# Kernel tuning notes

Measured on AMD Instinct MI355X. Metric: run time of the kernel, lower is better.

The kernel has to match this reference:

```python
import jax, jax.numpy as jnp
import numpy as np

EMBED_DIM = 128
NUM_HEADS = 16
D_K = EMBED_DIM // NUM_HEADS  # must equal n_wires = 8


def setup_inputs() -> dict:
    key = jax.random.key(0)
    k1, k2 = jax.random.split(key)
    x = jax.random.normal(k1, (8, 2048, EMBED_DIM), dtype=jnp.float32)
    theta = jax.random.normal(k2, (D_K,), dtype=jnp.float32)  # trainable RX angles, one per wire
    return {"x": x, "theta": theta}


def _quantum_measure(q, theta):
    # q: [B, H, S, 8]. RX(x)RX(theta) = RX(x+theta); product state gives <Z_i> = cos(phi_i).
    # CNOT chain C(0,1)..C(6,7),C(7,0) in Heisenberg picture:
    #   <Z_0> = prod_{i=1..7} cos(phi_i);  <Z_w> = prod_{i=0..w} cos(phi_i), w>=1.
    c = jnp.cos(q + theta)                       # [B,H,S,8]
    cp = jnp.cumprod(c, axis=-1)                 # prefix products prod_{0..w}
    z0 = jnp.prod(c[..., 1:], axis=-1, keepdims=True)
    return jnp.concatenate([z0, cp[..., 1:]], axis=-1)  # [B,H,S,8]


def reference(x, theta):
    B, S, E = x.shape
    # split heads: [B,S,E] -> [B,H,S,d_k]
    q = x.reshape(B, S, NUM_HEADS, D_K).transpose(0, 2, 1, 3)
    out = _quantum_measure(q, theta)             # [B,H,S,8]
    # merge heads back: [B,S,E]
    out = out.transpose(0, 2, 1, 3).reshape(B, S, E)
    scores = jnp.einsum('bse,bte->bst', out, out) / jnp.sqrt(jnp.float32(D_K))
    attn = jax.nn.softmax(scores, axis=-1)       # dropout = identity in eval mode
    return jnp.einsum('bst,bte->bse', attn, out)
```

## Files before the change

### kernel.cpp

```cpp
#include <hip/hip_runtime.h>

#define NB 8
#define SS 2048
#define DD 128
#define SCALE2 0.5101817664764817f
#define NEGINF -3.0e38f

typedef _Float16 f16x8 __attribute__((ext_vector_type(8)));
typedef float f32x16 __attribute__((ext_vector_type(16)));
typedef unsigned short u16;
typedef u16 u16x8 __attribute__((ext_vector_type(8)));
typedef unsigned int u32;

__device__ __forceinline__ u32 pkrtz(float a, float b) {
    u32 w;
    asm("v_cvt_pkrtz_f16_f32 %0, %1, %2" : "=v"(w) : "v"(a), "v"(b));
    return w;
}

__device__ __forceinline__ void gload_lds16(const u16* g, u16* l) {
    __builtin_amdgcn_global_load_lds(
        (const __attribute__((address_space(1))) unsigned*)g,
        (__attribute__((address_space(3))) unsigned*)l, 16, 0, 0);
}

__global__ __launch_bounds__(512) void qmeasure_kernel(const float* __restrict__ x,
                                                       const float* __restrict__ theta,
                                                       u16* __restrict__ G1,
                                                       u16* __restrict__ G2) {
    __shared__ u16 olds[32][136];
    const int bid = blockIdx.x;
    const int b = bid & 7;
    const int t = bid >> 3;
    const int tid = threadIdx.x;
    const int s = tid >> 4;
    const int c = tid & 15;

    float th[8];
    *(float4*)th = *(const float4*)theta;
    *(float4*)(th + 4) = *(const float4*)(theta + 4);

    const float* xp = x + (((size_t)b * SS + t * 32 + s) * DD) + c * 8;
    float4 a = *(const float4*)xp;
    float4 a2 = *(const float4*)(xp + 4);
    float cc[8];
    cc[0] = __cosf(a.x + th[0]);  cc[1] = __cosf(a.y + th[1]);
    cc[2] = __cosf(a.z + th[2]);  cc[3] = __cosf(a.w + th[3]);
    cc[4] = __cosf(a2.x + th[4]); cc[5] = __cosf(a2.y + th[5]);
    cc[6] = __cosf(a2.z + th[6]); cc[7] = __cosf(a2.w + th[7]);
    float o[8];
    o[1] = cc[0] * cc[1];
    o[2] = o[1] * cc[2]; o[3] = o[2] * cc[3]; o[4] = o[3] * cc[4];
    o[5] = o[4] * cc[5]; o[6] = o[5] * cc[6]; o[7] = o[6] * cc[7];
    float z = cc[1] * cc[2]; z *= cc[3]; z *= cc[4]; z *= cc[5]; z *= cc[6]; z *= cc[7];
    o[0] = z;

    u16x8 w;
#pragma unroll
    for (int e = 0; e < 8; ++e) w[e] = __builtin_bit_cast(u16, (_Float16)o[e]);
    *(u16x8*)&olds[s][c * 8] = w;
    __syncthreads();

    {
        const int kc = tid >> 6, hh = (tid >> 5) & 1, r = tid & 31;
        u16x8 g;
#pragma unroll
        for (int u = 0; u < 8; ++u) g[u] = olds[r][kc * 16 + hh * 8 + u];
        *(u16x8*)(G1 + (size_t)b * (SS * DD) + ((size_t)t * 512 + tid) * 8) = g;
    }
    {
        const int lo5 = tid & 31;
        const int hh = (tid >> 5) & 1;
        const int dkc = tid >> 6;
        const int dt = dkc >> 1, kc2 = dkc & 1;
        u16x8 g;
#pragma unroll
        for (int u = 0; u < 8; ++u) g[u] = olds[kc2 * 16 + hh * 8 + u][dt * 32 + lo5];
        const int chunk = t * 512 + dkc * 64 + hh * 32 + lo5;
        *(u16x8*)(G2 + (size_t)b * (SS * DD) + (size_t)chunk * 8) = g;
    }
}

__global__ __launch_bounds__(512, 2) void qattn_kernel(const u16* __restrict__ G1g,
                                                       const u16* __restrict__ G2g,
                                                       float* __restrict__ out) {
    __shared__ __align__(16) u16 sb[2][2][4][4096];

    const int tid = threadIdx.x;
    const int lane = tid & 63;
    const int wave = tid >> 6;
    const int lo5 = lane & 31;
    const int hi = lane >> 5;
    const int qw = wave & 1;
    const int kq = wave >> 1;
    const int bid = blockIdx.x;
    const int b = bid & 7;
    const int qg = bid >> 3;

    const u16* G1b = G1g + (size_t)b * (SS * DD);
    const u16* G2b = G2g + (size_t)b * (SS * DD);
    const u16* sbase = (qw ? G2b : G1b);

    f16x8 qf[8];
    {
        const u16* qp = G1b + (size_t)(qg * 2 + qw) * 4096 + lane * 8;
#pragma unroll
        for (int kc = 0; kc < 8; ++kc) qf[kc] = *(const f16x8*)(qp + kc * 512);
    }

#pragma unroll
    for (int pb = 0; pb < 2; ++pb) {
        const u16* src = sbase + (size_t)(kq * 16 + pb) * 4096 + lane * 8;
        u16* dst = &sb[pb][qw][kq][0];
#pragma unroll
        for (int w = 0; w < 8; ++w) gload_lds16(src + w * 512, dst + w * 512);
    }

    f32x16 accT[4];
#pragma unroll
    for (int dt = 0; dt < 4; ++dt)
#pragma unroll
        for (int e = 0; e < 16; ++e) accT[dt][e] = 0.f;
    float m = NEGINF, l = 0.f;

    for (int it = 0; it < 16; ++it) {
        const int cur = it & 1;
        if (it < 15) asm volatile("s_waitcnt vmcnt(8)" ::: "memory");
        else         asm volatile("s_waitcnt vmcnt(0)" ::: "memory");
        __builtin_amdgcn_sched_barrier(0);
        __builtin_amdgcn_s_barrier();
        __builtin_amdgcn_sched_barrier(0);

        const u16* Kb = &sb[cur][0][kq][0] + lane * 8;
        const u16* Vb = &sb[cur][1][kq][0] + lane * 8;

        f32x16 acA, acB;
#pragma unroll
        for (int e = 0; e < 16; ++e) { acA[e] = 0.f; acB[e] = 0.f; }
        __builtin_amdgcn_s_setprio(1);
#pragma unroll
        for (int kc = 0; kc < 4; ++kc) {
            f16x8 kf = *(const f16x8*)(Kb + kc * 512);
            acA = __builtin_amdgcn_mfma_f32_32x32x16_f16(kf, qf[kc], acA, 0, 0, 0);
        }
#pragma unroll
        for (int kc = 4; kc < 8; ++kc) {
            f16x8 kf = *(const f16x8*)(Kb + kc * 512);
            acB = __builtin_amdgcn_mfma_f32_32x32x16_f16(kf, qf[kc], acB, 0, 0, 0);
        }
        __builtin_amdgcn_s_setprio(0);
        f32x16 acc = acA + acB;

        f16x8 vf[8];
#pragma unroll
        for (int j = 0; j < 8; ++j) vf[j] = *(const f16x8*)(Vb + j * 512);

        float ma = fmaxf(fmaxf(acc[0], acc[1]), acc[2]);
        float mb = fmaxf(fmaxf(acc[8], acc[9]), acc[10]);
        ma = fmaxf(fmaxf(ma, acc[3]), acc[4]);
        mb = fmaxf(fmaxf(mb, acc[11]), acc[12]);
        ma = fmaxf(fmaxf(ma, acc[5]), acc[6]);
        mb = fmaxf(fmaxf(mb, acc[13]), acc[14]);
        ma = fmaxf(fmaxf(ma, acc[7]), mb);
        float tmax = fmaxf(ma, acc[15]) * SCALE2;
        tmax = fmaxf(tmax, __shfl_xor(tmax, 32));
        if (!__all(tmax <= m + 8.f)) {
            const float mnew = fmaxf(m, tmax);
            const float corr = exp2f(m - mnew);
            l *= corr;
#pragma unroll
            for (int dt = 0; dt < 4; ++dt)
#pragma unroll
                for (int e = 0; e < 16; ++e) accT[dt][e] *= corr;
            m = mnew;
        }
#pragma unroll
        for (int r = 0; r < 16; ++r) acc[r] = exp2f(acc[r] * SCALE2 - m);
        float s0 = (acc[0] + acc[1]) + (acc[2] + acc[3]);
        float s1 = (acc[4] + acc[5]) + (acc[6] + acc[7]);
        float s2 = (acc[8] + acc[9]) + (acc[10] + acc[11]);
        float s3 = (acc[12] + acc[13]) + (acc[14] + acc[15]);
        float rowsum = (s0 + s1) + (s2 + s3);
        rowsum += __shfl_xor(rowsum, 32);
        l += rowsum;

        f16x8 pa[2];
#pragma unroll
        for (int kc2 = 0; kc2 < 2; ++kc2) {
            const int r0 = kc2 * 8;
            u32 w0 = pkrtz(acc[r0 + 0], acc[r0 + 1]);
            u32 w2 = pkrtz(acc[r0 + 4], acc[r0 + 5]);
            asm("v_permlane32_swap_b32 %0, %1" : "+v"(w0), "+v"(w2));
            u32 w1 = pkrtz(acc[r0 + 2], acc[r0 + 3]);
            u32 w3 = pkrtz(acc[r0 + 6], acc[r0 + 7]);
            asm("v_permlane32_swap_b32 %0, %1" : "+v"(w1), "+v"(w3));
            union { u32 w[4]; f16x8 v; } u;
            u.w[0] = w0; u.w[1] = w1; u.w[2] = w2; u.w[3] = w3;
            pa[kc2] = u.v;
        }

        __builtin_amdgcn_s_setprio(1);
#pragma unroll
        for (int dt = 0; dt < 4; ++dt) {
            f32x16 a = accT[dt];
            a = __builtin_amdgcn_mfma_f32_32x32x16_f16(vf[dt * 2 + 0], pa[0], a, 0, 0, 0);
            a = __builtin_amdgcn_mfma_f32_32x32x16_f16(vf[dt * 2 + 1], pa[1], a, 0, 0, 0);
            accT[dt] = a;
        }
        __builtin_amdgcn_s_setprio(0);

        asm volatile("s_waitcnt lgkmcnt(0)" ::: "memory");
        __builtin_amdgcn_sched_barrier(0);
        __builtin_amdgcn_s_barrier();
        __builtin_amdgcn_sched_barrier(0);

        if (it < 14) {
            const u16* src = sbase + (size_t)(kq * 16 + it + 2) * 4096 + lane * 8;
            u16* dst = &sb[cur][qw][kq][0];
#pragma unroll
            for (int w = 0; w < 8; ++w) gload_lds16(src + w * 512, dst + w * 512);
        }
    }

    __syncthreads();
    float* obuf = (float*)(&sb[0][0][0][0]);
    float* mlb = (float*)((unsigned char*)(&sb[0][0][0][0]) + 49152);
    float* orow = out + ((size_t)b * SS + qg * 64 + qw * 32 + lo5) * DD;
#pragma unroll
    for (int half = 0; half < 2; ++half) {
        if (kq > 0) {
            if (half == 0 && hi == 0) {
                mlb[((qw * 3 + (kq - 1)) * 2 + 0) * 32 + lo5] = m;
                mlb[((qw * 3 + (kq - 1)) * 2 + 1) * 32 + lo5] = l;
            }
#pragma unroll
            for (int dh = 0; dh < 2; ++dh)
#pragma unroll
                for (int r = 0; r < 16; ++r)
                    obuf[(((qw * 3 + (kq - 1)) * 2 + dh) * 16 + r) * 64 + lane] =
                        accT[half * 2 + dh][r];
        }
        __syncthreads();
        if (kq == 0) {
            const float mj0 = mlb[((qw * 3 + 0) * 2 + 0) * 32 + lo5];
            const float lj0 = mlb[((qw * 3 + 0) * 2 + 1) * 32 + lo5];
            const float mj1 = mlb[((qw * 3 + 1) * 2 + 0) * 32 + lo5];
            const float lj1 = mlb[((qw * 3 + 1) * 2 + 1) * 32 + lo5];
            const float mj2 = mlb[((qw * 3 + 2) * 2 + 0) * 32 + lo5];
            const float lj2 = mlb[((qw * 3 + 2) * 2 + 1) * 32 + lo5];
            const float ms = fmaxf(fmaxf(m, mj0), fmaxf(mj1, mj2));
            const float w0 = exp2f(m - ms), w1 = exp2f(mj0 - ms);
            const float w2 = exp2f(mj1 - ms), w3 = exp2f(mj2 - ms);
            const float linv = 1.f / (l * w0 + lj0 * w1 + lj1 * w2 + lj2 * w3);
#pragma unroll
            for (int dh = 0; dh < 2; ++dh) {
                const int dt = half * 2 + dh;
#pragma unroll
                for (int r = 0; r < 16; ++r) {
                    const float o = accT[dt][r] * w0 +
                                    obuf[(((qw * 3 + 0) * 2 + dh) * 16 + r) * 64 + lane] * w1 +
                                    obuf[(((qw * 3 + 1) * 2 + dh) * 16 + r) * 64 + lane] * w2 +
                                    obuf[(((qw * 3 + 2) * 2 + dh) * 16 + r) * 64 + lane] * w3;
                    const int drow = (r & 3) + 8 * (r >> 2) + 4 * hi;
                    orow[dt * 32 + drow] = o * linv;
                }
            }
        }
        __syncthreads();
    }
}

extern "C" void kernel_launch(void* const* d_in, const int* in_sizes, int n_in,
                              void* d_out, int out_size, void* d_ws, size_t ws_size,
                              hipStream_t stream) {
    const float* x = (const float*)d_in[0];
    const float* theta = (const float*)d_in[1];
    float* outp = (float*)d_out;
    u16* G1 = (u16*)d_ws;
    u16* G2 = G1 + (size_t)NB * SS * DD;

    qmeasure_kernel<<<512, 512, 0, stream>>>(x, theta, G1, G2);
    qattn_kernel<<<256, 512, 0, stream>>>(G1, G2, outp);
}
```

Before: 40.66 us.

## Load K tiles into registers and give each wave private V buffers without barriers

K tiles now go straight from global memory into register double buffers (kfA/kfB), and V tiles are staged in LDS buffers private to each wave. Before, both were shared LDS tiles that paired waves loaded cooperatively. Each wave now fetches its own K and V, so the per-iteration block-wide s_barriers and lgkmcnt waits disappear and the loop is unrolled by two with software prefetch. The cost is duplicated global loads, since both query waves read the same K/V, plus higher VGPR pressure from 16 K fragments held in registers. LDS use doubles to 128 KB, which may cut occupancy below the declared 2 blocks per CU.

```diff
diff --git a/kernel.cpp b/kernel.cpp
--- a/kernel.cpp
+++ b/kernel.cpp
@@ -81,10 +81,90 @@
     }
 }
 
+template <bool LAST>
+__device__ __forceinline__ void attn_step(const f16x8* __restrict__ kf,
+                                          const u16* __restrict__ vlds, int lane8,
+                                          const f16x8* __restrict__ qf,
+                                          f32x16* __restrict__ accT,
+                                          float& m, float& l) {
+    f32x16 acA, acB;
+#pragma unroll
+    for (int e = 0; e < 16; ++e) { acA[e] = 0.f; acB[e] = 0.f; }
+    __builtin_amdgcn_s_setprio(1);
+#pragma unroll
+    for (int kc = 0; kc < 4; ++kc)
+        acA = __builtin_amdgcn_mfma_f32_32x32x16_f16(kf[kc], qf[kc], acA, 0, 0, 0);
+#pragma unroll
+    for (int kc = 4; kc < 8; ++kc)
+        acB = __builtin_amdgcn_mfma_f32_32x32x16_f16(kf[kc], qf[kc], acB, 0, 0, 0);
+    __builtin_amdgcn_s_setprio(0);
+    f32x16 acc = acA + acB;
+
+    float ma = fmaxf(fmaxf(acc[0], acc[1]), acc[2]);
+    float mb = fmaxf(fmaxf(acc[8], acc[9]), acc[10]);
+    ma = fmaxf(fmaxf(ma, acc[3]), acc[4]);
+    mb = fmaxf(fmaxf(mb, acc[11]), acc[12]);
+    ma = fmaxf(fmaxf(ma, acc[5]), acc[6]);
+    mb = fmaxf(fmaxf(mb, acc[13]), acc[14]);
+    ma = fmaxf(fmaxf(ma, acc[7]), mb);
+    float tmax = fmaxf(ma, acc[15]) * SCALE2;
+    tmax = fmaxf(tmax, __shfl_xor(tmax, 32));
+    if (!__all(tmax <= m + 8.f)) {
+        const float mnew = fmaxf(m, tmax);
+        const float corr = exp2f(m - mnew);
+        l *= corr;
+#pragma unroll
+        for (int dt = 0; dt < 4; ++dt)
+#pragma unroll
+            for (int e = 0; e < 16; ++e) accT[dt][e] *= corr;
+        m = mnew;
+    }
+#pragma unroll
+    for (int r = 0; r < 16; ++r) acc[r] = exp2f(acc[r] * SCALE2 - m);
+    float s0 = (acc[0] + acc[1]) + (acc[2] + acc[3]);
+    float s1 = (acc[4] + acc[5]) + (acc[6] + acc[7]);
+    float s2 = (acc[8] + acc[9]) + (acc[10] + acc[11]);
+    float s3 = (acc[12] + acc[13]) + (acc[14] + acc[15]);
+    float rowsum = (s0 + s1) + (s2 + s3);
+    rowsum += __shfl_xor(rowsum, 32);
+    l += rowsum;
+
+    f16x8 pa[2];
+#pragma unroll
+    for (int kc2 = 0; kc2 < 2; ++kc2) {
+        const int r0 = kc2 * 8;
+        u32 w0 = pkrtz(acc[r0 + 0], acc[r0 + 1]);
+        u32 w2 = pkrtz(acc[r0 + 4], acc[r0 + 5]);
+        asm("v_permlane32_swap_b32 %0, %1" : "+v"(w0), "+v"(w2));
+        u32 w1 = pkrtz(acc[r0 + 2], acc[r0 + 3]);
+        u32 w3 = pkrtz(acc[r0 + 6], acc[r0 + 7]);
+        asm("v_permlane32_swap_b32 %0, %1" : "+v"(w1), "+v"(w3));
+        union { u32 w[4]; f16x8 v; } u;
+        u.w[0] = w0; u.w[1] = w1; u.w[2] = w2; u.w[3] = w3;
+        pa[kc2] = u.v;
+    }
+
+    if (LAST) asm volatile("s_waitcnt vmcnt(0)" ::: "memory");
+    else      asm volatile("s_waitcnt vmcnt(16)" ::: "memory");
+    __builtin_amdgcn_sched_barrier(0);
+
+    __builtin_amdgcn_s_setprio(1);
+#pragma unroll
+    for (int dt = 0; dt < 4; ++dt) {
+        f16x8 vf0 = *(const f16x8*)(vlds + (dt * 2 + 0) * 512 + lane8);
+        f16x8 vf1 = *(const f16x8*)(vlds + (dt * 2 + 1) * 512 + lane8);
+        f32x16 a = accT[dt];
+        a = __builtin_amdgcn_mfma_f32_32x32x16_f16(vf0, pa[0], a, 0, 0, 0);
+        a = __builtin_amdgcn_mfma_f32_32x32x16_f16(vf1, pa[1], a, 0, 0, 0);
+        accT[dt] = a;
+    }
+    __builtin_amdgcn_s_setprio(0);
+}
+
 __global__ __launch_bounds__(512, 2) void qattn_kernel(const u16* __restrict__ G1g,
                                                        const u16* __restrict__ G2g,
                                                        float* __restrict__ out) {
-    __shared__ __align__(16) u16 sb[2][2][4][4096];
+    __shared__ __align__(16) u16 vbuf[2][8][4096];
 
     const int tid = threadIdx.x;
     const int lane = tid & 63;
@@ -96,24 +176,16 @@
     const int bid = blockIdx.x;
     const int b = bid & 7;
     const int qg = bid >> 3;
+    const int lane8 = lane * 8;
 
     const u16* G1b = G1g + (size_t)b * (SS * DD);
     const u16* G2b = G2g + (size_t)b * (SS * DD);
-    const u16* sbase = (qw ? G2b : G1b);
 
     f16x8 qf[8];
     {
-        const u16* qp = G1b + (size_t)(qg * 2 + qw) * 4096 + lane * 8;
+        const u16* qp = G1b + (size_t)(qg * 2 + qw) * 4096 + lane8;
 #pragma unroll
         for (int kc = 0; kc < 8; ++kc) qf[kc] = *(const f16x8*)(qp + kc * 512);
-    }
-
-#pragma unroll
-    for (int pb = 0; pb < 2; ++pb) {
-        const u16* src = sbase + (size_t)(kq * 16 + pb) * 4096 + lane * 8;
-        u16* dst = &sb[pb][qw][kq][0];
-#pragma unroll
-        for (int w = 0; w < 8; ++w) gload_lds16(src + w * 512, dst + w * 512);
     }
 
     f32x16 accT[4];
@@ -123,108 +195,54 @@
         for (int e = 0; e < 16; ++e) accT[dt][e] = 0.f;
     float m = NEGINF, l = 0.f;
 
-    for (int it = 0; it < 16; ++it) {
-        const int cur = it & 1;
-        if (it < 15) asm volatile("s_waitcnt vmcnt(8)" ::: "memory");
-        else         asm volatile("s_waitcnt vmcnt(0)" ::: "memory");
+    u16* const myv0 = &vbuf[0][wave][0];
+    u16* const myv1 = &vbuf[1][wave][0];
+
+    {
+        const u16* vsrc = G2b + (size_t)(kq * 16) * 4096 + lane8;
         __builtin_amdgcn_sched_barrier(0);
-        __builtin_amdgcn_s_barrier();
+#pragma unroll
+        for (int w = 0; w < 8; ++w) gload_lds16(vsrc + w * 512, myv0 + w * 512);
         __builtin_amdgcn_sched_barrier(0);
-
-        const u16* Kb = &sb[cur][0][kq][0] + lane * 8;
-        const u16* Vb = &sb[cur][1][kq][0] + lane * 8;
-
-        f32x16 acA, acB;
-#pragma unroll
-        for (int e = 0; e < 16; ++e) { acA[e] = 0.f; acB[e] = 0.f; }
-        __builtin_amdgcn_s_setprio(1);
-#pragma unroll
-        for (int kc = 0; kc < 4; ++kc) {
-            f16x8 kf = *(const f16x8*)(Kb + kc * 512);
-            acA = __builtin_amdgcn_mfma_f32_32x32x16_f16(kf, qf[kc], acA, 0, 0, 0);
+    }
+    f16x8 kfA[8], kfB[8];
+    {
+        const u16* kp = G1b + (size_t)(kq * 16) * 4096 + lane8;
+#pragma unroll
+        for (int j = 0; j < 8; ++j) kfA[j] = *(const f16x8*)(kp + j * 512);
+    }
+
+    for (int it2 = 0; it2 < 8; ++it2) {
+        const int t = kq * 16 + it2 * 2;
+        {
+            const u16* vsrc = G2b + (size_t)(t + 1) * 4096 + lane8;
+            __builtin_amdgcn_sched_barrier(0);
+#pragma unroll
+            for (int w = 0; w < 8; ++w) gload_lds16(vsrc + w * 512, myv1 + w * 512);
+            __builtin_amdgcn_sched_barrier(0);
+            const u16* np = G1b + (size_t)(t + 1) * 4096 + lane8;
+#pragma unroll
+            for (int j = 0; j < 8; ++j) kfB[j] = *(const f16x8*)(np + j * 512);
+            attn_step<false>(kfA, myv0, lane8, qf, accT, m, l);
         }
-#pragma unroll
-        for (int kc = 4; kc < 8; ++kc) {
-            f16x8 kf = *(const f16x8*)(Kb + kc * 512);
-            acB = __builtin_amdgcn_mfma_f32_32x32x16_f16(kf, qf[kc], acB, 0, 0, 0);
+        if (it2 < 7) {
+            const u16* vsrc = G2b + (size_t)(t + 2) * 4096 + lane8;
+            __builtin_amdgcn_sched_barrier(0);
+#pragma unroll
+            for (int w = 0; w < 8; ++w) gload_lds16(vsrc + w * 512, myv0 + w * 512);
+            __builtin_amdgcn_sched_barrier(0);
+            const u16* np = G1b + (size_t)(t + 2) * 4096 + lane8;
+#pragma unroll
+            for (int j = 0; j < 8; ++j) kfA[j] = *(const f16x8*)(np + j * 512);
+            attn_step<false>(kfB, myv1, lane8, qf, accT, m, l);
+        } else {
+            attn_step<true>(kfB, myv1, lane8, qf, accT, m, l);
         }
-        __builtin_amdgcn_s_setprio(0);
-        f32x16 acc = acA + acB;
-
-        f16x8 vf[8];
-#pragma unroll
-        for (int j = 0; j < 8; ++j) vf[j] = *(const f16x8*)(Vb + j * 512);
-
-        float ma = fmaxf(fmaxf(acc[0], acc[1]), acc[2]);
-        float mb = fmaxf(fmaxf(acc[8], acc[9]), acc[10]);
-        ma = fmaxf(fmaxf(ma, acc[3]), acc[4]);
-        mb = fmaxf(fmaxf(mb, acc[11]), acc[12]);
-        ma = fmaxf(fmaxf(ma, acc[5]), acc[6]);
-        mb = fmaxf(fmaxf(mb, acc[13]), acc[14]);
-        ma = fmaxf(fmaxf(ma, acc[7]), mb);
-        float tmax = fmaxf(ma, acc[15]) * SCALE2;
-        tmax = fmaxf(tmax, __shfl_xor(tmax, 32));
-        if (!__all(tmax <= m + 8.f)) {
-            const float mnew = fmaxf(m, tmax);
-            const float corr = exp2f(m - mnew);
-            l *= corr;
-#pragma unroll
-            for (int dt = 0; dt < 4; ++dt)
-#pragma unroll
-                for (int e = 0; e < 16; ++e) accT[dt][e] *= corr;
-            m = mnew;
-        }
-#pragma unroll
-        for (int r = 0; r < 16; ++r) acc[r] = exp2f(acc[r] * SCALE2 - m);
-        float s0 = (acc[0] + acc[1]) + (acc[2] + acc[3]);
-        float s1 = (acc[4] + acc[5]) + (acc[6] + acc[7]);
-        float s2 = (acc[8] + acc[9]) + (acc[10] + acc[11]);
-        float s3 = (acc[12] + acc[13]) + (acc[14] + acc[15]);
-        float rowsum = (s0 + s1) + (s2 + s3);
-        rowsum += __shfl_xor(rowsum, 32);
-        l += rowsum;
-
-        f16x8 pa[2];
-#pragma unroll
-        for (int kc2 = 0; kc2 < 2; ++kc2) {
-            const int r0 = kc2 * 8;
-            u32 w0 = pkrtz(acc[r0 + 0], acc[r0 + 1]);
-            u32 w2 = pkrtz(acc[r0 + 4], acc[r0 + 5]);
-            asm("v_permlane32_swap_b32 %0, %1" : "+v"(w0), "+v"(w2));
-            u32 w1 = pkrtz(acc[r0 + 2], acc[r0 + 3]);
-            u32 w3 = pkrtz(acc[r0 + 6], acc[r0 + 7]);
-            asm("v_permlane32_swap_b32 %0, %1" : "+v"(w1), "+v"(w3));
-            union { u32 w[4]; f16x8 v; } u;
-            u.w[0] = w0; u.w[1] = w1; u.w[2] = w2; u.w[3] = w3;
-            pa[kc2] = u.v;
-        }
-
-        __builtin_amdgcn_s_setprio(1);
-#pragma unroll
-        for (int dt = 0; dt < 4; ++dt) {
-            f32x16 a = accT[dt];
-            a = __builtin_amdgcn_mfma_f32_32x32x16_f16(vf[dt * 2 + 0], pa[0], a, 0, 0, 0);
-            a = __builtin_amdgcn_mfma_f32_32x32x16_f16(vf[dt * 2 + 1], pa[1], a, 0, 0, 0);
-            accT[dt] = a;
-        }
-        __builtin_amdgcn_s_setprio(0);
-
-        asm volatile("s_waitcnt lgkmcnt(0)" ::: "memory");
-        __builtin_amdgcn_sched_barrier(0);
-        __builtin_amdgcn_s_barrier();
-        __builtin_amdgcn_sched_barrier(0);
-
-        if (it < 14) {
-            const u16* src = sbase + (size_t)(kq * 16 + it + 2) * 4096 + lane * 8;
-            u16* dst = &sb[cur][qw][kq][0];
-#pragma unroll
-            for (int w = 0; w < 8; ++w) gload_lds16(src + w * 512, dst + w * 512);
-        }
     }
 
     __syncthreads();
-    float* obuf = (float*)(&sb[0][0][0][0]);
-    float* mlb = (float*)((unsigned char*)(&sb[0][0][0][0]) + 49152);
+    float* obuf = (float*)(&vbuf[0][0][0]);
+    float* mlb = (float*)((unsigned char*)(&vbuf[0][0][0]) + 49152);
     float* orow = out + ((size_t)b * SS + qg * 64 + qw * 32 + lo5) * DD;
 #pragma unroll
     for (int half = 0; half < 2; ++half) {
```

Measured after the change: 59.77 us. 47.0% more time.
